# Performance work log

Hardware: AMD Instinct MI355X
Metric: run time of the kernel (lower is better)

## Reference

```python
import jax, jax.numpy as jnp
import numpy as np

L, P = 8, 512
HID = 128
N_COARSE, N_FINE = 64, 128
LVIS_NEAR, LVIS_FAR = 1e-3, 0.5
S = 100.0  # 1 / fixed_s_recp


def _mlp_sdf(x, w0, b0, w1, b1, w2, b2, w3, b3):
    # x: [..., 3] -> sdf [...]
    h = jax.nn.relu(x @ w0 + b0)
    h = jax.nn.relu(h @ w1 + b1)
    h = jax.nn.relu(h @ w2 + b2)
    return (h @ w3 + b3)[..., 0]


def _sdf_to_w(sdf, s):
    # faithful to sdf_to_w: cdf -> alpha -> visibility weights via cumprod
    cdf = jax.nn.sigmoid(sdf * s)
    alpha = jnp.clip((cdf[..., :-1] - cdf[..., 1:]) / (cdf[..., :-1] + 1e-10), 0.0, None)
    ones = jnp.ones(alpha.shape[:-1] + (1,), alpha.dtype)
    shifted = jnp.concatenate([ones, 1.0 - alpha + 1e-10], axis=-1)
    return alpha * jnp.cumprod(shifted, axis=-1)[..., :-1]


def _sample_pdf(bins, weights, u):
    # standard NeRF importance sampling; bins [...,M+1], weights [...,M], u [...,N]
    weights = weights + 1e-5
    pdf = weights / jnp.sum(weights, axis=-1, keepdims=True)
    cdf = jnp.cumsum(pdf, axis=-1)
    cdf = jnp.concatenate([jnp.zeros_like(cdf[..., :1]), cdf], axis=-1)  # [...,M+1]
    # searchsorted (right) via broadcast compare: [...,N,M+1]
    inds = jnp.sum((u[..., None] >= cdf[..., None, :]).astype(jnp.int32), axis=-1)
    below = jnp.clip(inds - 1, 0, cdf.shape[-1] - 1)
    above = jnp.clip(inds, 0, cdf.shape[-1] - 1)
    cdf_b = jnp.take_along_axis(cdf, below, axis=-1)
    cdf_a = jnp.take_along_axis(cdf, above, axis=-1)
    bins_b = jnp.take_along_axis(bins, below, axis=-1)
    bins_a = jnp.take_along_axis(bins, above, axis=-1)
    denom = cdf_a - cdf_b
    denom = jnp.where(denom < 1e-5, jnp.ones_like(denom), denom)
    t = (u - cdf_b) / denom
    return bins_b + t * (bins_a - bins_b)


def setup_inputs() -> dict:
    key = jax.random.key(0)
    ks = jax.random.split(key, 8)

    def lin(k, fi, fo):
        return jax.random.normal(k, (fi, fo), jnp.float32) / jnp.sqrt(jnp.float32(fi))

    return {
        "pts": jax.random.normal(ks[0], (1, P, 3), jnp.float32) * 0.5,
        "light_posi": jax.random.normal(ks[1], (L, 3), jnp.float32) * 2.0,
        "u": jax.random.uniform(ks[2], (L, P, N_FINE), jnp.float32),
        "w0": lin(ks[3], 3, HID), "b0": jnp.zeros((HID,), jnp.float32),
        "w1": lin(ks[4], HID, HID), "b1": jnp.zeros((HID,), jnp.float32),
        "w2": lin(ks[5], HID, HID), "b2": jnp.zeros((HID,), jnp.float32),
        "w3": lin(ks[6], HID, 1), "b3": jnp.zeros((1,), jnp.float32),
    }


def reference(pts, light_posi, u, w0, b0, w1, b1, w2, b2, w3, b3):
    sdf = lambda x: _mlp_sdf(x, w0, b0, w1, b1, w2, b2, w3, b3)
    # pts: [1,P,3]; light_posi: [L,3]
    pts2l = light_posi[:, None, :] - pts  # [L,P,3]
    pts2l = pts2l / jnp.linalg.norm(pts2l, axis=-1, keepdims=True)
    t = jnp.linspace(0.0, 1.0 - 1.0 / N_COARSE, N_COARSE, dtype=jnp.float32)
    d_coarse = LVIS_NEAR * (1.0 - t) + LVIS_FAR * t  # [N_COARSE]
    d_coarse = jnp.broadcast_to(d_coarse, (pts2l.shape[0], pts.shape[1], N_COARSE))
    # coarse sample points: [L,P,Nc,3]
    pts_coarse = pts[:, :, None, :] + d_coarse[..., None] * pts2l[:, :, None, :]
    w_coarse = _sdf_to_w(sdf(pts_coarse), S)  # [L,P,Nc-1]
    d_fine = _sample_pdf(d_coarse, w_coarse, u)  # [L,P,Nf]
    d_all = jnp.sort(jnp.concatenate([d_coarse, d_fine], axis=-1), axis=-1)  # [L,P,Nc+Nf]
    pts_all = pts[:, :, None, :] + d_all[..., None] * pts2l[:, :, None, :]
    w_all = _sdf_to_w(sdf(pts_all), S)
    occu = jnp.sum(w_all, axis=-1)  # [L,P]
    return 1.0 - occu
```

## Files before the change

kernel.cpp:

```cpp
#include <hip/hip_runtime.h>
#include <math.h>

#define NL 8
#define NP 512
#define NC 64
#define NF 128
#define NALL 192
#define NRAY (NL * NP)
#define HID 128

typedef _Float16 half8 __attribute__((ext_vector_type(8)));
typedef _Float16 half4v __attribute__((ext_vector_type(4)));
typedef float floatx16 __attribute__((ext_vector_type(16)));
typedef unsigned long long ull;

#define MFMA(a, b, c) __builtin_amdgcn_mfma_f32_32x32x16_f16((a), (b), (c), 0, 0, 0)

__device__ __forceinline__ float dcoarse_at(int i) {
    float t = (float)i * 0.015625f;
    return 1e-3f * (1.0f - t) + 0.5f * t;
}

__device__ __forceinline__ floatx16 fzero16() {
    floatx16 z;
#pragma unroll
    for (int i = 0; i < 16; ++i) z[i] = 0.f;
    return z;
}
__device__ __forceinline__ half8 hzero8() {
    half8 z;
#pragma unroll
    for (int i = 0; i < 8; ++i) z[i] = (_Float16)0.f;
    return z;
}

__global__ void prep_kernel(const float* __restrict__ w1, const float* __restrict__ w2,
                            _Float16* __restrict__ Wsp) {
    int f = blockIdx.x * 256 + threadIdx.x;
    int layer = blockIdx.y;
    const float* w = layer ? w2 : w1;
    int i = f & 7, l31 = (f >> 3) & 31, lhi = (f >> 8) & 1, ks = (f >> 9) & 7, jb = f >> 12;
    int j = jb * 32 + l31;
    int k = ks * 16 + lhi * 8 + i;
    float v = w[k * 128 + j];
    _Float16 hi = (_Float16)v;
    Wsp[(layer * 2 + 0) * 16384 + f] = hi;
    Wsp[(layer * 2 + 1) * 16384 + f] = (_Float16)(v - (float)hi);
}

template<int MODE, int FASTW>
__global__ __launch_bounds__(256, 2) void mlp_kernel(
    const float* __restrict__ pts, const float* __restrict__ lights,
    const float* __restrict__ u,
    float* __restrict__ d_fine, unsigned char* __restrict__ perm8,
    const float* __restrict__ w0, const float* __restrict__ b0,
    const float* __restrict__ w1, const float* __restrict__ b1,
    const float* __restrict__ w2, const float* __restrict__ b2,
    const float* __restrict__ w3, const float* __restrict__ b3,
    const _Float16* __restrict__ Wsp,
    float* __restrict__ sdf_c, float* __restrict__ out)
{
    __shared__ __align__(16) _Float16 Hhi[128 * 128];
    __shared__ __align__(16) _Float16 Hlo[128 * 128];
    __shared__ _Float16 Xs[6 * 128];
    __shared__ float P2[2 * 128];

    const int tid = threadIdx.x;
    const int lane = tid & 63;
    const int wv = tid >> 6;
    const int jh = wv & 1, mh = wv >> 1;
    const int l31 = lane & 31, lhi = lane >> 5;
    const int base = blockIdx.x * 128;

    if (tid < 128) {
        int pt = base + tid;
        int ray; float d;
        if (MODE == 0) { ray = pt >> 6; d = dcoarse_at(pt & 63); }
        else           { ray = pt >> 7; d = d_fine[pt]; }
        int l = ray >> 9, p = ray & (NP - 1);
        float px = pts[p * 3 + 0], py = pts[p * 3 + 1], pz = pts[p * 3 + 2];
        float dx = lights[l * 3 + 0] - px, dy = lights[l * 3 + 1] - py, dz = lights[l * 3 + 2] - pz;
        float n = sqrtf(dx * dx + dy * dy + dz * dz);
        dx /= n; dy /= n; dz /= n;
        float xc[3] = { px + d * dx, py + d * dy, pz + d * dz };
#pragma unroll
        for (int c = 0; c < 3; ++c) {
            _Float16 h = (_Float16)xc[c];
            Xs[c * 128 + tid] = h;
            Xs[(3 + c) * 128 + tid] = (_Float16)(xc[c] - (float)h);
        }
    }
    __syncthreads();

    const int m0 = mh * 64;

    auto haddr = [&](int m, int k0) {
        return m * 128 + ((((k0 >> 3) ^ (m & 15)) << 3) | (k0 & 7));
    };

    auto store_tile = [&](const floatx16& a, int jt, int mt, const float* __restrict__ bias) {
        int m = m0 + mt * 32 + l31;
#pragma unroll
        for (int g = 0; g < 4; ++g) {
            int jg = jh * 64 + jt * 32 + 8 * g + 4 * lhi;
            half4v hq, lq;
#pragma unroll
            for (int q = 0; q < 4; ++q) {
                float v = fmaxf(a[g * 4 + q] + bias[jg + q], 0.f);
                _Float16 hi = (_Float16)v;
                hq[q] = hi;
                lq[q] = (_Float16)(v - (float)hi);
            }
            int ad = haddr(m, jg);
            *(half4v*)&Hhi[ad] = hq;
            *(half4v*)&Hlo[ad] = lq;
        }
    };

    floatx16 acc[2][2];

    {
        half8 a1h[2], a1l[2], bh1[2], bl1[2];
#pragma unroll
        for (int jt = 0; jt < 2; ++jt) { a1h[jt] = hzero8(); a1l[jt] = hzero8(); }
#pragma unroll
        for (int mt = 0; mt < 2; ++mt) { bh1[mt] = hzero8(); bl1[mt] = hzero8(); }
        if (lhi == 0) {
#pragma unroll
            for (int jt = 0; jt < 2; ++jt) {
                int j = jh * 64 + jt * 32 + l31;
#pragma unroll
                for (int c = 0; c < 3; ++c) {
                    float v = w0[c * 128 + j];
                    _Float16 hi = (_Float16)v;
                    a1h[jt][c] = hi;
                    a1l[jt][c] = (_Float16)(v - (float)hi);
                }
            }
#pragma unroll
            for (int mt = 0; mt < 2; ++mt) {
                int m = m0 + mt * 32 + l31;
#pragma unroll
                for (int c = 0; c < 3; ++c) {
                    bh1[mt][c] = Xs[c * 128 + m];
                    bl1[mt][c] = Xs[(3 + c) * 128 + m];
                }
            }
        }
#pragma unroll
        for (int jt = 0; jt < 2; ++jt)
#pragma unroll
            for (int mt = 0; mt < 2; ++mt) acc[jt][mt] = fzero16();
#pragma unroll
        for (int jt = 0; jt < 2; ++jt)
#pragma unroll
            for (int mt = 0; mt < 2; ++mt) acc[jt][mt] = MFMA(a1l[jt], bh1[mt], acc[jt][mt]);
#pragma unroll
        for (int jt = 0; jt < 2; ++jt)
#pragma unroll
            for (int mt = 0; mt < 2; ++mt) acc[jt][mt] = MFMA(a1h[jt], bl1[mt], acc[jt][mt]);
#pragma unroll
        for (int jt = 0; jt < 2; ++jt)
#pragma unroll
            for (int mt = 0; mt < 2; ++mt) acc[jt][mt] = MFMA(a1h[jt], bh1[mt], acc[jt][mt]);
#pragma unroll
        for (int jt = 0; jt < 2; ++jt)
#pragma unroll
            for (int mt = 0; mt < 2; ++mt) store_tile(acc[jt][mt], jt, mt, b0);
    }
    __syncthreads();

    auto ldA = [&](int L, int jt, int ks, half8& ah, half8& al) {
        if (FASTW) {
            int off = ((((jh * 2 + jt) * 8 + ks) * 2 + lhi) * 32 + l31) * 8;
            ah = *(const half8*)&Wsp[(L * 2 + 0) * 16384 + off];
            al = *(const half8*)&Wsp[(L * 2 + 1) * 16384 + off];
        } else {
            const float* w = L ? w2 : w1;
            int j = jh * 64 + jt * 32 + l31, k0 = ks * 16 + lhi * 8;
#pragma unroll
            for (int i = 0; i < 8; ++i) {
                float v = w[(k0 + i) * 128 + j];
                _Float16 hi = (_Float16)v;
                ah[i] = hi;
                al[i] = (_Float16)(v - (float)hi);
            }
        }
    };

    half8 bh[2][8], bl[2][8];

    auto gemm = [&](int L) {
#pragma unroll
        for (int mt = 0; mt < 2; ++mt) {
            int m = m0 + mt * 32 + l31;
#pragma unroll
            for (int ks = 0; ks < 8; ++ks) {
                int ad = haddr(m, ks * 16 + lhi * 8);
                bh[mt][ks] = *(const half8*)&Hhi[ad];
                bl[mt][ks] = *(const half8*)&Hlo[ad];
            }
        }
#pragma unroll
        for (int jt = 0; jt < 2; ++jt)
#pragma unroll
            for (int mt = 0; mt < 2; ++mt) acc[jt][mt] = fzero16();
#pragma unroll
        for (int ks = 0; ks < 8; ++ks) {
            half8 ah[2], al[2];
            ldA(L, 0, ks, ah[0], al[0]);
            ldA(L, 1, ks, ah[1], al[1]);
#pragma unroll
            for (int jt = 0; jt < 2; ++jt)
#pragma unroll
                for (int mt = 0; mt < 2; ++mt) acc[jt][mt] = MFMA(al[jt], bh[mt][ks], acc[jt][mt]);
#pragma unroll
            for (int jt = 0; jt < 2; ++jt)
#pragma unroll
                for (int mt = 0; mt < 2; ++mt) acc[jt][mt] = MFMA(ah[jt], bl[mt][ks], acc[jt][mt]);
#pragma unroll
            for (int jt = 0; jt < 2; ++jt)
#pragma unroll
                for (int mt = 0; mt < 2; ++mt) acc[jt][mt] = MFMA(ah[jt], bh[mt][ks], acc[jt][mt]);
        }
    };

    gemm(0);
    __syncthreads();
#pragma unroll
    for (int jt = 0; jt < 2; ++jt)
#pragma unroll
        for (int mt = 0; mt < 2; ++mt) store_tile(acc[jt][mt], jt, mt, b1);
    __syncthreads();

    gemm(1);
#pragma unroll
    for (int mt = 0; mt < 2; ++mt) {
        float p = 0.f;
#pragma unroll
        for (int jt = 0; jt < 2; ++jt)
#pragma unroll
            for (int g = 0; g < 4; ++g) {
                int jg = jh * 64 + jt * 32 + 8 * g + 4 * lhi;
#pragma unroll
                for (int q = 0; q < 4; ++q) {
                    float v = fmaxf(acc[jt][mt][g * 4 + q] + b2[jg + q], 0.f);
                    p = fmaf(v, w3[jg + q], p);
                }
            }
        p += __shfl_xor(p, 32);
        if (lane < 32) P2[jh * 128 + m0 + mt * 32 + l31] = p;
    }
    __syncthreads();
    if (tid < 128) {
        float s = b3[0] + P2[tid] + P2[128 + tid];
        if (MODE == 0) sdf_c[base + tid] = s;
        P2[tid] = s;
    }
    __syncthreads();

    if (MODE == 0) {
        if (wv < 2) {
            const int ray = blockIdx.x * 2 + wv;
            float sv = P2[wv * 64 + lane];
            float c = 1.0f / (1.0f + expf(-100.0f * sv));
            float cn = __shfl_down(c, 1);
            bool valid = lane < 63;
            float a = valid ? fmaxf((c - cn) / (c + 1e-10f), 0.f) : 0.f;
            float sh = valid ? (1.f - a + 1e-10f) : 1.f;
            float ps = sh;
#pragma unroll
            for (int off = 1; off < 64; off <<= 1) { float o = __shfl_up(ps, off); if (lane >= off) ps *= o; }
            float T = __shfl_up(ps, 1);
            if (lane == 0) T = 1.f;
            float w = valid ? (a * T + 1e-5f) : 0.f;
            float wsum = w;
#pragma unroll
            for (int off = 1; off < 64; off <<= 1) wsum += __shfl_xor(wsum, off);
            float pdf = w / wsum;
            float cs = pdf;
#pragma unroll
            for (int off = 1; off < 64; off <<= 1) { float o = __shfl_up(cs, off); if (lane >= off) cs += o; }
            float cdfv = __shfl_up(cs, 1);
            if (lane == 0) cdfv = 0.f;

            float df[2];
#pragma unroll
            for (int t = 0; t < 2; ++t) {
                float uu = u[ray * NF + t * 64 + lane];
                int lo = 0;
#pragma unroll
                for (int b = 32; b >= 1; b >>= 1) {
                    float cm = __shfl(cdfv, lo + b);
                    if (uu >= cm) lo += b;
                }
                int above = min(lo + 1, NC - 1);
                float cb = __shfl(cdfv, lo), ca = __shfl(cdfv, above);
                float bb = dcoarse_at(lo), ba = dcoarse_at(above);
                float denom = ca - cb;
                if (denom < 1e-5f) denom = 1.f;
                float tt = (uu - cb) / denom;
                df[t] = bb + tt * (ba - bb);
                d_fine[ray * 128 + t * 64 + lane] = df[t];
            }

            ull v[4];
            v[0] = ((ull)__float_as_uint(dcoarse_at(lane)) << 32) | (unsigned)lane;
            v[1] = ((ull)__float_as_uint(df[0]) << 32) | (unsigned)(64 + lane);
            v[2] = ((ull)__float_as_uint(df[1]) << 32) | (unsigned)(128 + lane);
            v[3] = ((ull)0x7F800000u << 32) | 255u;
            for (int k = 2; k <= 256; k <<= 1) {
                for (int j = k >> 1; j > 0; j >>= 1) {
                    if (j >= 64) {
                        int tj = j >> 6;
#pragma unroll
                        for (int t = 0; t < 4; ++t) {
                            if ((t & tj) == 0) {
                                int t2 = t ^ tj;
                                bool asc = (((t * 64) & k) == 0);
                                ull x = v[t], y = v[t2];
                                bool sw = asc ? (x > y) : (x < y);
                                if (sw) { v[t] = y; v[t2] = x; }
                            }
                        }
                    } else {
#pragma unroll
                        for (int t = 0; t < 4; ++t) {
                            int i = t * 64 + lane;
                            ull other = __shfl_xor(v[t], j);
                            bool lower = (lane & j) == 0;
                            bool asc = ((i & k) == 0);
                            bool takeMin = (lower == asc);
                            ull mn = v[t] < other ? v[t] : other;
                            ull mx = v[t] < other ? other : v[t];
                            v[t] = takeMin ? mn : mx;
                        }
                    }
                }
            }
#pragma unroll
            for (int t = 0; t < 3; ++t)
                perm8[ray * NALL + t * 64 + lane] = (unsigned char)(v[t] & 0xFFu);
        }
    } else {
        if (wv == 0) {
            const int ray = blockIdx.x;
            const unsigned char* P = perm8 + (size_t)ray * NALL;
            float c[4];
#pragma unroll
            for (int t = 0; t < 4; ++t) {
                int i = lane * 3 + t;
                if (i < NALL) {
                    int idx = P[i];
                    float s = (idx < 64) ? sdf_c[ray * NC + idx] : P2[idx - 64];
                    c[t] = 1.0f / (1.0f + expf(-100.0f * s));
                } else c[t] = 0.f;
            }
            float a[3], s[3];
#pragma unroll
            for (int t = 0; t < 3; ++t) {
                int i = lane * 3 + t;
                if (i < NALL - 1) {
                    a[t] = fmaxf((c[t] - c[t + 1]) / (c[t] + 1e-10f), 0.f);
                    s[t] = 1.f - a[t] + 1e-10f;
                } else { a[t] = 0.f; s[t] = 1.f; }
            }
            float chunk = s[0] * s[1] * s[2];
            float ps = chunk;
#pragma unroll
            for (int off = 1; off < 64; off <<= 1) {
                float o = __shfl_up(ps, off);
                if (lane >= off) ps *= o;
            }
            float T = __shfl_up(ps, 1);
            if (lane == 0) T = 1.f;
            float occ = a[0] * T;
            T *= s[0]; occ = fmaf(a[1], T, occ);
            T *= s[1]; occ = fmaf(a[2], T, occ);
#pragma unroll
            for (int off = 1; off < 64; off <<= 1) occ += __shfl_xor(occ, off);
            if (lane == 0) out[ray] = 1.f - occ;
        }
    }
}

extern "C" void kernel_launch(void* const* d_in, const int* in_sizes, int n_in,
                              void* d_out, int out_size, void* d_ws, size_t ws_size,
                              hipStream_t stream) {
    const float* pts = (const float*)d_in[0];
    const float* lights = (const float*)d_in[1];
    const float* u = (const float*)d_in[2];
    const float* w0 = (const float*)d_in[3];
    const float* b0 = (const float*)d_in[4];
    const float* w1 = (const float*)d_in[5];
    const float* b1 = (const float*)d_in[6];
    const float* w2 = (const float*)d_in[7];
    const float* b2 = (const float*)d_in[8];
    const float* w3 = (const float*)d_in[9];
    const float* b3 = (const float*)d_in[10];
    float* out = (float*)d_out;

    char* wsb = (char*)d_ws;
    float* sdf_c = (float*)wsb;
    float* d_fine = (float*)(wsb + (size_t)NRAY * NC * 4);
    unsigned char* perm8 = (unsigned char*)(wsb + (size_t)NRAY * (NC + 128) * 4);
    _Float16* Wsp = (_Float16*)(wsb + (size_t)NRAY * (NC + 128) * 4 + (size_t)NRAY * NALL);
    const size_t need = (size_t)NRAY * (NC + 128) * 4 + (size_t)NRAY * NALL
                      + (size_t)4 * 16384 * sizeof(_Float16);
    const bool fast = ws_size >= need;

    if (fast) {
        prep_kernel<<<dim3(64, 2), 256, 0, stream>>>(w1, w2, Wsp);
        mlp_kernel<0, 1><<<(NRAY * NC) / 128, 256, 0, stream>>>(
            pts, lights, u, d_fine, perm8,
            w0, b0, w1, b1, w2, b2, w3, b3, Wsp, sdf_c, out);
        mlp_kernel<1, 1><<<NRAY, 256, 0, stream>>>(
            pts, lights, u, d_fine, perm8,
            w0, b0, w1, b1, w2, b2, w3, b3, Wsp, sdf_c, out);
    } else {
        mlp_kernel<0, 0><<<(NRAY * NC) / 128, 256, 0, stream>>>(
            pts, lights, u, d_fine, perm8,
            w0, b0, w1, b1, w2, b2, w3, b3, nullptr, sdf_c, out);
        mlp_kernel<1, 0><<<NRAY, 256, 0, stream>>>(
            pts, lights, u, d_fine, perm8,
            w0, b0, w1, b1, w2, b2, w3, b3, nullptr, sdf_c, out);
    }
}
```

Before: 279.4 us.

## Fuse coarse and fine MLP passes into one per-ray-pair kernel

Merges the coarse-sample MLP kernel and the fine-sample MLP kernel into a single kernel in which each block handles two rays over three rounds: coarse points first, then the fine points of each ray. SDF values, fine depths and the sort permutation now stay in shared memory instead of going through global workspace, which removes one launch and the global round trips between the two passes. In exchange each block runs serially through three dependent rounds with extra syncs. The grid also shrinks from 4096 blocks to 2048, so there is less parallelism for hiding latency.

```diff
diff --git a/kernel.cpp b/kernel.cpp
--- a/kernel.cpp
+++ b/kernel.cpp
@@ -48,55 +48,40 @@
     Wsp[(layer * 2 + 1) * 16384 + f] = (_Float16)(v - (float)hi);
 }
 
-template<int MODE, int FASTW>
-__global__ __launch_bounds__(256, 2) void mlp_kernel(
+template<int FASTW>
+__global__ __launch_bounds__(256, 2) void mega_kernel(
     const float* __restrict__ pts, const float* __restrict__ lights,
     const float* __restrict__ u,
-    float* __restrict__ d_fine, unsigned char* __restrict__ perm8,
     const float* __restrict__ w0, const float* __restrict__ b0,
     const float* __restrict__ w1, const float* __restrict__ b1,
     const float* __restrict__ w2, const float* __restrict__ b2,
     const float* __restrict__ w3, const float* __restrict__ b3,
     const _Float16* __restrict__ Wsp,
-    float* __restrict__ sdf_c, float* __restrict__ out)
+    float* __restrict__ out)
 {
     __shared__ __align__(16) _Float16 Hhi[128 * 128];
     __shared__ __align__(16) _Float16 Hlo[128 * 128];
     __shared__ _Float16 Xs[6 * 128];
     __shared__ float P2[2 * 128];
+    __shared__ float sdfC[128];
+    __shared__ float sdfF[256];
+    __shared__ float dF[256];
+    __shared__ unsigned char perm[2 * NALL];
 
     const int tid = threadIdx.x;
     const int lane = tid & 63;
     const int wv = tid >> 6;
     const int jh = wv & 1, mh = wv >> 1;
     const int l31 = lane & 31, lhi = lane >> 5;
-    const int base = blockIdx.x * 128;
-
-    if (tid < 128) {
-        int pt = base + tid;
-        int ray; float d;
-        if (MODE == 0) { ray = pt >> 6; d = dcoarse_at(pt & 63); }
-        else           { ray = pt >> 7; d = d_fine[pt]; }
-        int l = ray >> 9, p = ray & (NP - 1);
-        float px = pts[p * 3 + 0], py = pts[p * 3 + 1], pz = pts[p * 3 + 2];
-        float dx = lights[l * 3 + 0] - px, dy = lights[l * 3 + 1] - py, dz = lights[l * 3 + 2] - pz;
-        float n = sqrtf(dx * dx + dy * dy + dz * dz);
-        dx /= n; dy /= n; dz /= n;
-        float xc[3] = { px + d * dx, py + d * dy, pz + d * dz };
-#pragma unroll
-        for (int c = 0; c < 3; ++c) {
-            _Float16 h = (_Float16)xc[c];
-            Xs[c * 128 + tid] = h;
-            Xs[(3 + c) * 128 + tid] = (_Float16)(xc[c] - (float)h);
-        }
-    }
-    __syncthreads();
-
+    const int rayA = blockIdx.x * 2;
     const int m0 = mh * 64;
 
     auto haddr = [&](int m, int k0) {
         return m * 128 + ((((k0 >> 3) ^ (m & 15)) << 3) | (k0 & 7));
     };
+
+    floatx16 acc[2][2];
+    half8 bh[2][8], bl[2][8];
 
     auto store_tile = [&](const floatx16& a, int jt, int mt, const float* __restrict__ bias) {
         int m = m0 + mt * 32 + l31;
@@ -116,59 +101,6 @@
             *(half4v*)&Hlo[ad] = lq;
         }
     };
-
-    floatx16 acc[2][2];
-
-    {
-        half8 a1h[2], a1l[2], bh1[2], bl1[2];
-#pragma unroll
-        for (int jt = 0; jt < 2; ++jt) { a1h[jt] = hzero8(); a1l[jt] = hzero8(); }
-#pragma unroll
-        for (int mt = 0; mt < 2; ++mt) { bh1[mt] = hzero8(); bl1[mt] = hzero8(); }
-        if (lhi == 0) {
-#pragma unroll
-            for (int jt = 0; jt < 2; ++jt) {
-                int j = jh * 64 + jt * 32 + l31;
-#pragma unroll
-                for (int c = 0; c < 3; ++c) {
-                    float v = w0[c * 128 + j];
-                    _Float16 hi = (_Float16)v;
-                    a1h[jt][c] = hi;
-                    a1l[jt][c] = (_Float16)(v - (float)hi);
-                }
-            }
-#pragma unroll
-            for (int mt = 0; mt < 2; ++mt) {
-                int m = m0 + mt * 32 + l31;
-#pragma unroll
-                for (int c = 0; c < 3; ++c) {
-                    bh1[mt][c] = Xs[c * 128 + m];
-                    bl1[mt][c] = Xs[(3 + c) * 128 + m];
-                }
-            }
-        }
-#pragma unroll
-        for (int jt = 0; jt < 2; ++jt)
-#pragma unroll
-            for (int mt = 0; mt < 2; ++mt) acc[jt][mt] = fzero16();
-#pragma unroll
-        for (int jt = 0; jt < 2; ++jt)
-#pragma unroll
-            for (int mt = 0; mt < 2; ++mt) acc[jt][mt] = MFMA(a1l[jt], bh1[mt], acc[jt][mt]);
-#pragma unroll
-        for (int jt = 0; jt < 2; ++jt)
-#pragma unroll
-            for (int mt = 0; mt < 2; ++mt) acc[jt][mt] = MFMA(a1h[jt], bl1[mt], acc[jt][mt]);
-#pragma unroll
-        for (int jt = 0; jt < 2; ++jt)
-#pragma unroll
-            for (int mt = 0; mt < 2; ++mt) acc[jt][mt] = MFMA(a1h[jt], bh1[mt], acc[jt][mt]);
-#pragma unroll
-        for (int jt = 0; jt < 2; ++jt)
-#pragma unroll
-            for (int mt = 0; mt < 2; ++mt) store_tile(acc[jt][mt], jt, mt, b0);
-    }
-    __syncthreads();
 
     auto ldA = [&](int L, int jt, int ks, half8& ah, half8& al) {
         if (FASTW) {
@@ -188,8 +120,6 @@
         }
     };
 
-    half8 bh[2][8], bl[2][8];
-
     auto gemm = [&](int L) {
 #pragma unroll
         for (int mt = 0; mt < 2; ++mt) {
@@ -225,162 +155,235 @@
         }
     };
 
-    gemm(0);
-    __syncthreads();
-#pragma unroll
-    for (int jt = 0; jt < 2; ++jt)
-#pragma unroll
-        for (int mt = 0; mt < 2; ++mt) store_tile(acc[jt][mt], jt, mt, b1);
-    __syncthreads();
-
-    gemm(1);
-#pragma unroll
-    for (int mt = 0; mt < 2; ++mt) {
-        float p = 0.f;
+#pragma unroll 1
+    for (int rnd = 0; rnd < 3; ++rnd) {
+        if (tid < 128) {
+            int ray; float d;
+            if (rnd == 0) { ray = rayA + (tid >> 6); d = dcoarse_at(tid & 63); }
+            else          { ray = rayA + (rnd - 1);  d = dF[(rnd - 1) * 128 + tid]; }
+            int l = ray >> 9, p = ray & (NP - 1);
+            float px = pts[p * 3 + 0], py = pts[p * 3 + 1], pz = pts[p * 3 + 2];
+            float dx = lights[l * 3 + 0] - px, dy = lights[l * 3 + 1] - py, dz = lights[l * 3 + 2] - pz;
+            float n = sqrtf(dx * dx + dy * dy + dz * dz);
+            dx /= n; dy /= n; dz /= n;
+            float xc[3] = { px + d * dx, py + d * dy, pz + d * dz };
+#pragma unroll
+            for (int c = 0; c < 3; ++c) {
+                _Float16 h = (_Float16)xc[c];
+                Xs[c * 128 + tid] = h;
+                Xs[(3 + c) * 128 + tid] = (_Float16)(xc[c] - (float)h);
+            }
+        }
+        __syncthreads();
+
+        {
+            half8 a1h[2], a1l[2], bh1[2], bl1[2];
+#pragma unroll
+            for (int jt = 0; jt < 2; ++jt) { a1h[jt] = hzero8(); a1l[jt] = hzero8(); }
+#pragma unroll
+            for (int mt = 0; mt < 2; ++mt) { bh1[mt] = hzero8(); bl1[mt] = hzero8(); }
+            if (lhi == 0) {
+#pragma unroll
+                for (int jt = 0; jt < 2; ++jt) {
+                    int j = jh * 64 + jt * 32 + l31;
+#pragma unroll
+                    for (int c = 0; c < 3; ++c) {
+                        float v = w0[c * 128 + j];
+                        _Float16 hi = (_Float16)v;
+                        a1h[jt][c] = hi;
+                        a1l[jt][c] = (_Float16)(v - (float)hi);
+                    }
+                }
+#pragma unroll
+                for (int mt = 0; mt < 2; ++mt) {
+                    int m = m0 + mt * 32 + l31;
+#pragma unroll
+                    for (int c = 0; c < 3; ++c) {
+                        bh1[mt][c] = Xs[c * 128 + m];
+                        bl1[mt][c] = Xs[(3 + c) * 128 + m];
+                    }
+                }
+            }
+#pragma unroll
+            for (int jt = 0; jt < 2; ++jt)
+#pragma unroll
+                for (int mt = 0; mt < 2; ++mt) acc[jt][mt] = fzero16();
+#pragma unroll
+            for (int jt = 0; jt < 2; ++jt)
+#pragma unroll
+                for (int mt = 0; mt < 2; ++mt) acc[jt][mt] = MFMA(a1l[jt], bh1[mt], acc[jt][mt]);
+#pragma unroll
+            for (int jt = 0; jt < 2; ++jt)
+#pragma unroll
+                for (int mt = 0; mt < 2; ++mt) acc[jt][mt] = MFMA(a1h[jt], bl1[mt], acc[jt][mt]);
+#pragma unroll
+            for (int jt = 0; jt < 2; ++jt)
+#pragma unroll
+                for (int mt = 0; mt < 2; ++mt) acc[jt][mt] = MFMA(a1h[jt], bh1[mt], acc[jt][mt]);
+#pragma unroll
+            for (int jt = 0; jt < 2; ++jt)
+#pragma unroll
+                for (int mt = 0; mt < 2; ++mt) store_tile(acc[jt][mt], jt, mt, b0);
+        }
+        __syncthreads();
+
+        gemm(0);
+        __syncthreads();
 #pragma unroll
         for (int jt = 0; jt < 2; ++jt)
 #pragma unroll
-            for (int g = 0; g < 4; ++g) {
-                int jg = jh * 64 + jt * 32 + 8 * g + 4 * lhi;
-#pragma unroll
-                for (int q = 0; q < 4; ++q) {
-                    float v = fmaxf(acc[jt][mt][g * 4 + q] + b2[jg + q], 0.f);
-                    p = fmaf(v, w3[jg + q], p);
+            for (int mt = 0; mt < 2; ++mt) store_tile(acc[jt][mt], jt, mt, b1);
+        __syncthreads();
+
+        gemm(1);
+#pragma unroll
+        for (int mt = 0; mt < 2; ++mt) {
+            float p = 0.f;
+#pragma unroll
+            for (int jt = 0; jt < 2; ++jt)
+#pragma unroll
+                for (int g = 0; g < 4; ++g) {
+                    int jg = jh * 64 + jt * 32 + 8 * g + 4 * lhi;
+#pragma unroll
+                    for (int q = 0; q < 4; ++q) {
+                        float v = fmaxf(acc[jt][mt][g * 4 + q] + b2[jg + q], 0.f);
+                        p = fmaf(v, w3[jg + q], p);
+                    }
                 }
-            }
-        p += __shfl_xor(p, 32);
-        if (lane < 32) P2[jh * 128 + m0 + mt * 32 + l31] = p;
-    }
-    __syncthreads();
-    if (tid < 128) {
-        float s = b3[0] + P2[tid] + P2[128 + tid];
-        if (MODE == 0) sdf_c[base + tid] = s;
-        P2[tid] = s;
-    }
-    __syncthreads();
-
-    if (MODE == 0) {
-        if (wv < 2) {
-            const int ray = blockIdx.x * 2 + wv;
-            float sv = P2[wv * 64 + lane];
-            float c = 1.0f / (1.0f + expf(-100.0f * sv));
-            float cn = __shfl_down(c, 1);
-            bool valid = lane < 63;
-            float a = valid ? fmaxf((c - cn) / (c + 1e-10f), 0.f) : 0.f;
-            float sh = valid ? (1.f - a + 1e-10f) : 1.f;
-            float ps = sh;
-#pragma unroll
-            for (int off = 1; off < 64; off <<= 1) { float o = __shfl_up(ps, off); if (lane >= off) ps *= o; }
-            float T = __shfl_up(ps, 1);
-            if (lane == 0) T = 1.f;
-            float w = valid ? (a * T + 1e-5f) : 0.f;
-            float wsum = w;
-#pragma unroll
-            for (int off = 1; off < 64; off <<= 1) wsum += __shfl_xor(wsum, off);
-            float pdf = w / wsum;
-            float cs = pdf;
-#pragma unroll
-            for (int off = 1; off < 64; off <<= 1) { float o = __shfl_up(cs, off); if (lane >= off) cs += o; }
-            float cdfv = __shfl_up(cs, 1);
-            if (lane == 0) cdfv = 0.f;
-
-            float df[2];
-#pragma unroll
-            for (int t = 0; t < 2; ++t) {
-                float uu = u[ray * NF + t * 64 + lane];
-                int lo = 0;
-#pragma unroll
-                for (int b = 32; b >= 1; b >>= 1) {
-                    float cm = __shfl(cdfv, lo + b);
-                    if (uu >= cm) lo += b;
+            p += __shfl_xor(p, 32);
+            if (lane < 32) P2[jh * 128 + m0 + mt * 32 + l31] = p;
+        }
+        __syncthreads();
+        if (tid < 128) {
+            float s = b3[0] + P2[tid] + P2[128 + tid];
+            if (rnd == 0) sdfC[tid] = s;
+            else          sdfF[(rnd - 1) * 128 + tid] = s;
+        }
+        __syncthreads();
+
+        if (rnd == 0) {
+            if (wv < 2) {
+                const int ray = rayA + wv;
+                float sv = sdfC[wv * 64 + lane];
+                float c = 1.0f / (1.0f + expf(-100.0f * sv));
+                float cn = __shfl_down(c, 1);
+                bool valid = lane < 63;
+                float a = valid ? fmaxf((c - cn) / (c + 1e-10f), 0.f) : 0.f;
+                float sh = valid ? (1.f - a + 1e-10f) : 1.f;
+                float ps = sh;
+#pragma unroll
+                for (int off = 1; off < 64; off <<= 1) { float o = __shfl_up(ps, off); if (lane >= off) ps *= o; }
+                float T = __shfl_up(ps, 1);
+                if (lane == 0) T = 1.f;
+                float w = valid ? (a * T + 1e-5f) : 0.f;
+                float wsum = w;
+#pragma unroll
+                for (int off = 1; off < 64; off <<= 1) wsum += __shfl_xor(wsum, off);
+                float pdf = w / wsum;
+                float cs = pdf;
+#pragma unroll
+                for (int off = 1; off < 64; off <<= 1) { float o = __shfl_up(cs, off); if (lane >= off) cs += o; }
+                float cdfv = __shfl_up(cs, 1);
+                if (lane == 0) cdfv = 0.f;
+
+                float df[2];
+#pragma unroll
+                for (int t = 0; t < 2; ++t) {
+                    float uu = u[ray * NF + t * 64 + lane];
+                    int lo = 0;
+#pragma unroll
+                    for (int b = 32; b >= 1; b >>= 1) {
+                        float cm = __shfl(cdfv, lo + b);
+                        if (uu >= cm) lo += b;
+                    }
+                    int above = min(lo + 1, NC - 1);
+                    float cb = __shfl(cdfv, lo), ca = __shfl(cdfv, above);
+                    float bb = dcoarse_at(lo), ba = dcoarse_at(above);
+                    float denom = ca - cb;
+                    if (denom < 1e-5f) denom = 1.f;
+                    float tt = (uu - cb) / denom;
+                    df[t] = bb + tt * (ba - bb);
+                    dF[wv * 128 + t * 64 + lane] = df[t];
                 }
-                int above = min(lo + 1, NC - 1);
-                float cb = __shfl(cdfv, lo), ca = __shfl(cdfv, above);
-                float bb = dcoarse_at(lo), ba = dcoarse_at(above);
-                float denom = ca - cb;
-                if (denom < 1e-5f) denom = 1.f;
-                float tt = (uu - cb) / denom;
-                df[t] = bb + tt * (ba - bb);
-                d_fine[ray * 128 + t * 64 + lane] = df[t];
-            }
-
-            ull v[4];
-            v[0] = ((ull)__float_as_uint(dcoarse_at(lane)) << 32) | (unsigned)lane;
-            v[1] = ((ull)__float_as_uint(df[0]) << 32) | (unsigned)(64 + lane);
-            v[2] = ((ull)__float_as_uint(df[1]) << 32) | (unsigned)(128 + lane);
-            v[3] = ((ull)0x7F800000u << 32) | 255u;
-            for (int k = 2; k <= 256; k <<= 1) {
-                for (int j = k >> 1; j > 0; j >>= 1) {
-                    if (j >= 64) {
-                        int tj = j >> 6;
-#pragma unroll
-                        for (int t = 0; t < 4; ++t) {
-                            if ((t & tj) == 0) {
-                                int t2 = t ^ tj;
-                                bool asc = (((t * 64) & k) == 0);
-                                ull x = v[t], y = v[t2];
-                                bool sw = asc ? (x > y) : (x < y);
-                                if (sw) { v[t] = y; v[t2] = x; }
+
+                ull v[4];
+                v[0] = ((ull)__float_as_uint(dcoarse_at(lane)) << 32) | (unsigned)lane;
+                v[1] = ((ull)__float_as_uint(df[0]) << 32) | (unsigned)(64 + lane);
+                v[2] = ((ull)__float_as_uint(df[1]) << 32) | (unsigned)(128 + lane);
+                v[3] = ((ull)0x7F800000u << 32) | 255u;
+                for (int k = 2; k <= 256; k <<= 1) {
+                    for (int j = k >> 1; j > 0; j >>= 1) {
+                        if (j >= 64) {
+                            int tj = j >> 6;
+#pragma unroll
+                            for (int t = 0; t < 4; ++t) {
+                                if ((t & tj) == 0) {
+                                    int t2 = t ^ tj;
+                                    bool asc = (((t * 64) & k) == 0);
+                                    ull x = v[t], y = v[t2];
+                                    bool sw = asc ? (x > y) : (x < y);
+                                    if (sw) { v[t] = y; v[t2] = x; }
+                                }
                             }
-                        }
-                    } else {
-#pragma unroll
-                        for (int t = 0; t < 4; ++t) {
-                            int i = t * 64 + lane;
-                            ull other = __shfl_xor(v[t], j);
-                            bool lower = (lane & j) == 0;
-                            bool asc = ((i & k) == 0);
-                            bool takeMin = (lower == asc);
-                            ull mn = v[t] < other ? v[t] : other;
-                            ull mx = v[t] < other ? other : v[t];
-                            v[t] = takeMin ? mn : mx;
+                        } else {
+#pragma unroll
+                            for (int t = 0; t < 4; ++t) {
+                                int i = t * 64 + lane;
+                                ull other = __shfl_xor(v[t], j);
+                                bool lower = (lane & j) == 0;
+                                bool asc = ((i & k) == 0);
+                                bool takeMin = (lower == asc);
+                                ull mn = v[t] < other ? v[t] : other;
+                                ull mx = v[t] < other ? other : v[t];
+                                v[t] = takeMin ? mn : mx;
+                            }
                         }
                     }
                 }
-            }
-#pragma unroll
-            for (int t = 0; t < 3; ++t)
-                perm8[ray * NALL + t * 64 + lane] = (unsigned char)(v[t] & 0xFFu);
-        }
-    } else {
-        if (wv == 0) {
-            const int ray = blockIdx.x;
-            const unsigned char* P = perm8 + (size_t)ray * NALL;
-            float c[4];
-#pragma unroll
-            for (int t = 0; t < 4; ++t) {
-                int i = lane * 3 + t;
-                if (i < NALL) {
-                    int idx = P[i];
-                    float s = (idx < 64) ? sdf_c[ray * NC + idx] : P2[idx - 64];
-                    c[t] = 1.0f / (1.0f + expf(-100.0f * s));
-                } else c[t] = 0.f;
-            }
-            float a[3], s[3];
-#pragma unroll
-            for (int t = 0; t < 3; ++t) {
-                int i = lane * 3 + t;
-                if (i < NALL - 1) {
-                    a[t] = fmaxf((c[t] - c[t + 1]) / (c[t] + 1e-10f), 0.f);
-                    s[t] = 1.f - a[t] + 1e-10f;
-                } else { a[t] = 0.f; s[t] = 1.f; }
-            }
-            float chunk = s[0] * s[1] * s[2];
-            float ps = chunk;
-#pragma unroll
-            for (int off = 1; off < 64; off <<= 1) {
-                float o = __shfl_up(ps, off);
-                if (lane >= off) ps *= o;
-            }
-            float T = __shfl_up(ps, 1);
-            if (lane == 0) T = 1.f;
-            float occ = a[0] * T;
-            T *= s[0]; occ = fmaf(a[1], T, occ);
-            T *= s[1]; occ = fmaf(a[2], T, occ);
-#pragma unroll
-            for (int off = 1; off < 64; off <<= 1) occ += __shfl_xor(occ, off);
-            if (lane == 0) out[ray] = 1.f - occ;
-        }
+#pragma unroll
+                for (int t = 0; t < 3; ++t)
+                    perm[wv * NALL + t * 64 + lane] = (unsigned char)(v[t] & 0xFFu);
+            }
+            __syncthreads();
+        }
+    }
+
+    if (wv < 2) {
+        const unsigned char* P = perm + wv * NALL;
+        float c[4];
+#pragma unroll
+        for (int t = 0; t < 4; ++t) {
+            int i = lane * 3 + t;
+            if (i < NALL) {
+                int idx = P[i];
+                float s = (idx < 64) ? sdfC[wv * 64 + idx] : sdfF[wv * 128 + (idx - 64)];
+                c[t] = 1.0f / (1.0f + expf(-100.0f * s));
+            } else c[t] = 0.f;
+        }
+        float a[3], s[3];
+#pragma unroll
+        for (int t = 0; t < 3; ++t) {
+            int i = lane * 3 + t;
+            if (i < NALL - 1) {
+                a[t] = fmaxf((c[t] - c[t + 1]) / (c[t] + 1e-10f), 0.f);
+                s[t] = 1.f - a[t] + 1e-10f;
+            } else { a[t] = 0.f; s[t] = 1.f; }
+        }
+        float chunk = s[0] * s[1] * s[2];
+        float ps = chunk;
+#pragma unroll
+        for (int off = 1; off < 64; off <<= 1) {
+            float o = __shfl_up(ps, off);
+            if (lane >= off) ps *= o;
+        }
+        float T = __shfl_up(ps, 1);
+        if (lane == 0) T = 1.f;
+        float occ = a[0] * T;
+        T *= s[0]; occ = fmaf(a[1], T, occ);
+        T *= s[1]; occ = fmaf(a[2], T, occ);
+#pragma unroll
+        for (int off = 1; off < 64; off <<= 1) occ += __shfl_xor(occ, off);
+        if (lane == 0) out[rayA + wv] = 1.f - occ;
     }
 }
 
@@ -400,29 +403,15 @@
     const float* b3 = (const float*)d_in[10];
     float* out = (float*)d_out;
 
-    char* wsb = (char*)d_ws;
-    float* sdf_c = (float*)wsb;
-    float* d_fine = (float*)(wsb + (size_t)NRAY * NC * 4);
-    unsigned char* perm8 = (unsigned char*)(wsb + (size_t)NRAY * (NC + 128) * 4);
-    _Float16* Wsp = (_Float16*)(wsb + (size_t)NRAY * (NC + 128) * 4 + (size_t)NRAY * NALL);
-    const size_t need = (size_t)NRAY * (NC + 128) * 4 + (size_t)NRAY * NALL
-                      + (size_t)4 * 16384 * sizeof(_Float16);
-    const bool fast = ws_size >= need;
+    _Float16* Wsp = (_Float16*)d_ws;
+    const bool fast = ws_size >= (size_t)4 * 16384 * sizeof(_Float16);
 
     if (fast) {
         prep_kernel<<<dim3(64, 2), 256, 0, stream>>>(w1, w2, Wsp);
-        mlp_kernel<0, 1><<<(NRAY * NC) / 128, 256, 0, stream>>>(
-            pts, lights, u, d_fine, perm8,
-            w0, b0, w1, b1, w2, b2, w3, b3, Wsp, sdf_c, out);
-        mlp_kernel<1, 1><<<NRAY, 256, 0, stream>>>(
-            pts, lights, u, d_fine, perm8,
-            w0, b0, w1, b1, w2, b2, w3, b3, Wsp, sdf_c, out);
+        mega_kernel<1><<<NRAY / 2, 256, 0, stream>>>(
+            pts, lights, u, w0, b0, w1, b1, w2, b2, w3, b3, Wsp, out);
     } else {
-        mlp_kernel<0, 0><<<(NRAY * NC) / 128, 256, 0, stream>>>(
-            pts, lights, u, d_fine, perm8,
-            w0, b0, w1, b1, w2, b2, w3, b3, nullptr, sdf_c, out);
-        mlp_kernel<1, 0><<<NRAY, 256, 0, stream>>>(
-            pts, lights, u, d_fine, perm8,
-            w0, b0, w1, b1, w2, b2, w3, b3, nullptr, sdf_c, out);
+        mega_kernel<0><<<NRAY / 2, 256, 0, stream>>>(
+            pts, lights, u, w0, b0, w1, b1, w2, b2, w3, b3, nullptr, out);
     }
 }
```

Measured after the change: 567.0 us. 2.03x slower.
